# Performance work log

Hardware: AMD Instinct MI355X
Metric: run time of the kernel (lower is better)

The kernel has to match this reference:

```python
import jax, jax.numpy as jnp
import numpy as np

N = 65536          # nodes
E = 1048576        # edges
IN_C = 128
HID_C = 32
HEADS = 4
OUT_C = 64
NEG_SLOPE = 0.2
EPS = 1e-16


def gat_conv(x, edge_index, W, att_src, att_dst, bias, heads, out_c, concat):
    """PyG-style GATConv. x: [N, F_in]; edge_index: [2, E] (row=src, col=dst).
    W: [F_in, heads*out_c]; att_src/att_dst: [heads, out_c]; bias: [heads*out_c] or [out_c]."""
    src, dst = edge_index[0], edge_index[1]
    n = x.shape[0]
    h = (x @ W).reshape(n, heads, out_c)                      # [N, H, C]
    a_src = jnp.einsum('nhc,hc->nh', h, att_src)              # [N, H]
    a_dst = jnp.einsum('nhc,hc->nh', h, att_dst)              # [N, H]
    alpha = a_src[src] + a_dst[dst]                           # [E, H]
    alpha = jax.nn.leaky_relu(alpha, NEG_SLOPE)
    # segment softmax over incoming edges of each destination node
    amax = jax.ops.segment_max(alpha, dst, num_segments=n)    # [N, H]
    alpha = jnp.exp(alpha - amax[dst])
    denom = jax.ops.segment_sum(alpha, dst, num_segments=n)   # [N, H]
    alpha = alpha / (denom[dst] + EPS)
    # weighted scatter-add aggregation
    msgs = alpha[:, :, None] * h[src]                         # [E, H, C]
    out = jax.ops.segment_sum(msgs, dst, num_segments=n)      # [N, H, C]
    if concat:
        out = out.reshape(n, heads * out_c)
    else:
        out = out.mean(axis=1)
    return out + bias


def setup_inputs() -> dict:
    key = jax.random.key(0)
    ks = jax.random.split(key, 10)
    s_in = 1.0 / np.sqrt(IN_C)
    s_h = 1.0 / np.sqrt(HEADS * HID_C)
    x = jax.random.normal(ks[0], (N, IN_C), dtype=jnp.float32)
    edge_index = jax.random.randint(ks[1], (2, E), 0, N, dtype=jnp.int64)
    W1 = jax.random.normal(ks[2], (IN_C, HEADS * HID_C), dtype=jnp.float32) * s_in
    att_src1 = jax.random.normal(ks[3], (HEADS, HID_C), dtype=jnp.float32) * s_h
    att_dst1 = jax.random.normal(ks[4], (HEADS, HID_C), dtype=jnp.float32) * s_h
    b1 = jnp.zeros((HEADS * HID_C,), dtype=jnp.float32)
    W2 = jax.random.normal(ks[5], (HEADS * HID_C, OUT_C), dtype=jnp.float32) * s_h
    att_src2 = jax.random.normal(ks[6], (1, OUT_C), dtype=jnp.float32) * s_h
    att_dst2 = jax.random.normal(ks[7], (1, OUT_C), dtype=jnp.float32) * s_h
    b2 = jnp.zeros((OUT_C,), dtype=jnp.float32)
    return {"x": x, "edge_index": edge_index, "W1": W1, "att_src1": att_src1,
            "att_dst1": att_dst1, "b1": b1, "W2": W2, "att_src2": att_src2,
            "att_dst2": att_dst2, "b2": b2}


def reference(x, edge_index, W1, att_src1, att_dst1, b1, W2, att_src2, att_dst2, b2):
    # dropout is identity in eval mode
    h = gat_conv(x, edge_index, W1, att_src1, att_dst1, b1, HEADS, HID_C, concat=True)
    h = jax.nn.sigmoid(h)
    h = gat_conv(h, edge_index, W2, att_src2, att_dst2, b2, 1, OUT_C, concat=True)
    return jax.nn.sigmoid(h)
```

## Files before the change

kernel.cpp:

```cpp
#include <hip/hip_runtime.h>
#include <hip/hip_fp16.h>

#define N_NODES 65536
#define N_EDGES 1048576
#define NBUCK 256
#define PBLOCKS 1024
#define EPB (N_EDGES / PBLOCKS)
#define K4CAP 6144
#define GB1 (N_NODES / 64)
constexpr float NEG = 0.2f;
constexpr float EPS_ = 1e-16f;
constexpr float WSHIFT = 2.7725887f;

typedef __attribute__((ext_vector_type(8))) short bf16x8;
typedef __attribute__((ext_vector_type(4))) float f32x4;

__device__ __forceinline__ unsigned short f2bf(float f) {
    unsigned int u = __float_as_uint(f);
    return (unsigned short)((u + 0x7fffu + ((u >> 16) & 1u)) >> 16);
}
__device__ __forceinline__ unsigned short f2h(float f) {
    __half_raw r = __half_raw(__float2half(f));
    return r.x;
}
__device__ __forceinline__ __half2 u2h2(unsigned int u) {
    union { unsigned int u; __half2 h; } c; c.u = u; return c.h;
}
__device__ __forceinline__ unsigned int h22u(__half2 h) {
    union { unsigned int u; __half2 h; } c; c.h = h; return c.u;
}
__device__ __forceinline__ float lrelu_exp_s(float l) {
    return __expf(fmaxf(l, NEG * l) - WSHIFT);
}


__global__ __launch_bounds__(1024) void scan_a(const int* __restrict__ in,
                                               int* __restrict__ out,
                                               int* __restrict__ bsum) {
    __shared__ int sm[1024];
    int t = threadIdx.x, i = blockIdx.x * 1024 + t;
    int v = in[i];
    sm[t] = v;
    __syncthreads();
    for (int off = 1; off < 1024; off <<= 1) {
        int u = (t >= off) ? sm[t - off] : 0;
        __syncthreads();
        sm[t] += u;
        __syncthreads();
    }
    out[i] = sm[t] - v;
    if (t == 1023) bsum[blockIdx.x] = sm[t];
}

__global__ __launch_bounds__(1024) void scan_c(int* __restrict__ arr,
                                               const int* __restrict__ bsum) {
    __shared__ int partial[4];
    int t = threadIdx.x;
    if (t < 256) {
        int v = (t < (int)blockIdx.x) ? bsum[t] : 0;
        #pragma unroll
        for (int msk = 1; msk < 64; msk <<= 1) v += __shfl_xor(v, msk);
        if ((t & 63) == 0) partial[t >> 6] = v;
    }
    __syncthreads();
    int pref = partial[0] + partial[1] + partial[2] + partial[3];
    arr[blockIdx.x * 1024 + t] += pref;
}

__global__ __launch_bounds__(256) void partition_kernel(const int* __restrict__ ei,
                                                        const int* __restrict__ cursor_mat,
                                                        unsigned int* __restrict__ edge_part) {
    __shared__ int h[NBUCK];
    __shared__ int start[NBUCK];
    __shared__ int cur[NBUCK];
    __shared__ int gcur[NBUCK];
    __shared__ unsigned int stage[EPB];
    int t = threadIdx.x;
    h[t] = 0;
    gcur[t] = cursor_mat[t * PBLOCKS + blockIdx.x];
    __syncthreads();
    unsigned int ent[EPB / 256];
    int base = blockIdx.x * EPB;
    #pragma unroll
    for (int i = 0; i < EPB / 256; ++i) {
        int e = base + i * 256 + t;
        int s = ei[e], d = ei[N_EDGES + e];
        ent[i] = ((unsigned int)s << 16) | (unsigned int)d;
        atomicAdd(&h[d >> 8], 1);
    }
    __syncthreads();
    int v = h[t];
    start[t] = v;
    __syncthreads();
    for (int off = 1; off < 256; off <<= 1) {
        int u = (t >= off) ? start[t - off] : 0;
        __syncthreads();
        start[t] += u;
        __syncthreads();
    }
    int excl = start[t] - v;
    start[t] = excl;
    cur[t] = excl;
    __syncthreads();
    #pragma unroll
    for (int i = 0; i < EPB / 256; ++i) {
        int b = (int)((ent[i] & 0xffffu) >> 8);
        int slot = atomicAdd(&cur[b], 1);
        stage[slot] = ent[i];
    }
    __syncthreads();
    int s0 = t * (EPB / 256);
    #pragma unroll
    for (int i = 0; i < EPB / 256; ++i) {
        unsigned int p = stage[s0 + i];
        int b = (int)((p & 0xffffu) >> 8);
        edge_part[gcur[b] + (s0 + i - start[b])] = p;
    }
}

__global__ __launch_bounds__(1024) void finalize_kernel(const unsigned int* __restrict__ edge_part,
                                                        const int* __restrict__ cursor_mat,
                                                        int* __restrict__ row_ptr,
                                                        unsigned short* __restrict__ csr16) {
    __shared__ int h[256];
    __shared__ int sc[256];
    __shared__ int cur[256];
    __shared__ unsigned short stage[K4CAP];
    int t = threadIdx.x;
    int b = blockIdx.x;
    if (b == NBUCK - 1 && t == 0) row_ptr[N_NODES] = N_EDGES;
    int cs = cursor_mat[b * PBLOCKS];
    int ce = (b == NBUCK - 1) ? N_EDGES : cursor_mat[(b + 1) * PBLOCKS];
    int cnt = ce - cs;
    if (t < 256) h[t] = 0;
    __syncthreads();
    for (int i = t; i < cnt; i += 1024)
        atomicAdd(&h[edge_part[cs + i] & 0xffu], 1);
    __syncthreads();
    int v = 0;
    if (t < 256) { v = h[t]; sc[t] = v; }
    __syncthreads();
    for (int off = 1; off < 256; off <<= 1) {
        int u = (t < 256 && t >= off) ? sc[t - off] : 0;
        __syncthreads();
        if (t < 256) sc[t] += u;
        __syncthreads();
    }
    if (t < 256) {
        int excl = sc[t] - v;
        row_ptr[b * 256 + t] = cs + excl;
        cur[t] = excl;
    }
    __syncthreads();
    if (cnt <= K4CAP) {
        for (int i = t; i < cnt; i += 1024) {
            unsigned int p = edge_part[cs + i];
            int slot = atomicAdd(&cur[p & 0xffu], 1);
            stage[slot] = (unsigned short)(p >> 16);
        }
        __syncthreads();
        for (int i = t; i < cnt; i += 1024)
            csr16[cs + i] = stage[i];
    } else {
        for (int i = t; i < cnt; i += 1024) {
            unsigned int p = edge_part[cs + i];
            int slot = atomicAdd(&cur[p & 0xffu], 1);
            csr16[cs + slot] = (unsigned short)(p >> 16);
        }
    }
}


__global__ __launch_bounds__(256) void gemm1_hist(const float* __restrict__ X,
                                                  const float* __restrict__ W,
                                                  const float* __restrict__ as_w,
                                                  const float* __restrict__ ad_w,
                                                  const int* __restrict__ ei,
                                                  unsigned short* __restrict__ H,
                                                  float* __restrict__ a_src,
                                                  float* __restrict__ a_dst,
                                                  int* __restrict__ hist_mat) {
    extern __shared__ unsigned short Wl[];
    int t = threadIdx.x;
    if (blockIdx.x >= GB1) {
        int* hs = (int*)Wl;
        int pb = blockIdx.x - GB1;
        hs[t] = 0;
        __syncthreads();
        int base = pb * EPB;
        #pragma unroll
        for (int i = 0; i < EPB / 256; ++i) {
            int d = ei[N_EDGES + base + i * 256 + t];
            atomicAdd(&hs[d >> 8], 1);
        }
        __syncthreads();
        hist_mat[t * PBLOCKS + pb] = hs[t];
        return;
    }
    constexpr int OUTC = 128;
    constexpr int NT = OUTC / 16;
    for (int idx = t; idx < OUTC * 128; idx += 256) {
        int j = idx & 7;
        int ln = (idx >> 3) & 63;
        int fc = idx >> 9;
        int kc = fc & 3, ct = fc >> 2;
        int k = kc * 32 + (ln >> 4) * 8 + j;
        int nn = ct * 16 + (ln & 15);
        Wl[idx] = (unsigned short)f2bf(W[k * OUTC + nn]);
    }
    __syncthreads();
    int wave = t >> 6, lane = t & 63;
    int m = lane & 15, quad = lane >> 4;
    int node_base = blockIdx.x * 64 + wave * 16;
    const float* xrow = X + (size_t)(node_base + m) * 128 + quad * 8;
    bf16x8 a[4];
    #pragma unroll
    for (int kc = 0; kc < 4; ++kc) {
        float4 u = *(const float4*)(xrow + kc * 32);
        float4 v = *(const float4*)(xrow + kc * 32 + 4);
        bf16x8 af;
        af[0] = (short)f2bf(u.x); af[1] = (short)f2bf(u.y);
        af[2] = (short)f2bf(u.z); af[3] = (short)f2bf(u.w);
        af[4] = (short)f2bf(v.x); af[5] = (short)f2bf(v.y);
        af[6] = (short)f2bf(v.z); af[7] = (short)f2bf(v.w);
        a[kc] = af;
    }
    float asv[NT], adv[NT];
    #pragma unroll
    for (int ct = 0; ct < NT; ++ct) {
        asv[ct] = as_w[ct * 16 + m];
        adv[ct] = ad_w[ct * 16 + m];
    }
    float ps[4][4] = {};
    float pd[4][4] = {};
    #pragma unroll
    for (int ct = 0; ct < NT; ++ct) {
        f32x4 acc = {0.f, 0.f, 0.f, 0.f};
        #pragma unroll
        for (int kc = 0; kc < 4; ++kc) {
            bf16x8 bfr = *(const bf16x8*)(Wl + ((ct * 4 + kc) * 64 + lane) * 8);
            acc = __builtin_amdgcn_mfma_f32_16x16x32_bf16(a[kc], bfr, acc, 0, 0, 0);
        }
        int hh = ct >> 1;
        #pragma unroll
        for (int r = 0; r < 4; ++r) {
            H[(size_t)(node_base + quad * 4 + r) * OUTC + ct * 16 + m] = f2h(acc[r]);
            ps[r][hh] += acc[r] * asv[ct];
            pd[r][hh] += acc[r] * adv[ct];
        }
    }
    #pragma unroll
    for (int r = 0; r < 4; ++r) {
        #pragma unroll
        for (int hh = 0; hh < 4; ++hh) {
            float s = ps[r][hh], d = pd[r][hh];
            #pragma unroll
            for (int msk = 1; msk < 16; msk <<= 1) {
                s += __shfl_xor(s, msk);
                d += __shfl_xor(d, msk);
            }
            if (m == 0) {
                int node = node_base + quad * 4 + r;
                a_src[node * 4 + hh] = s;
                a_dst[node * 4 + hh] = d;
            }
        }
    }
}


__global__ __launch_bounds__(256) void gemm2_mfma(const unsigned short* __restrict__ X,
                                                  const float* __restrict__ W,
                                                  const float* __restrict__ as_w,
                                                  const float* __restrict__ ad_w,
                                                  unsigned short* __restrict__ H,
                                                  float* __restrict__ a_src,
                                                  float* __restrict__ a_dst) {
    constexpr int OUTC = 64;
    constexpr int NT = OUTC / 16;
    extern __shared__ unsigned short Wl[];
    int t = threadIdx.x;
    for (int idx = t; idx < OUTC * 128; idx += 256) {
        int j = idx & 7;
        int ln = (idx >> 3) & 63;
        int fc = idx >> 9;
        int kc = fc & 3, ct = fc >> 2;
        int k = kc * 32 + (ln >> 4) * 8 + j;
        int nn = ct * 16 + (ln & 15);
        Wl[idx] = (unsigned short)f2bf(W[k * OUTC + nn]);
    }
    __syncthreads();
    int wave = t >> 6, lane = t & 63;
    int m = lane & 15, quad = lane >> 4;
    int node_base = blockIdx.x * 64 + wave * 16;
    const unsigned short* xrow = X + (size_t)(node_base + m) * 128 + quad * 8;
    bf16x8 a[4];
    #pragma unroll
    for (int kc = 0; kc < 4; ++kc) a[kc] = *(const bf16x8*)(xrow + kc * 32);
    float asv[NT], adv[NT];
    #pragma unroll
    for (int ct = 0; ct < NT; ++ct) {
        asv[ct] = as_w[ct * 16 + m];
        adv[ct] = ad_w[ct * 16 + m];
    }
    float ps[4] = {};
    float pd[4] = {};
    #pragma unroll
    for (int ct = 0; ct < NT; ++ct) {
        f32x4 acc = {0.f, 0.f, 0.f, 0.f};
        #pragma unroll
        for (int kc = 0; kc < 4; ++kc) {
            bf16x8 bfr = *(const bf16x8*)(Wl + ((ct * 4 + kc) * 64 + lane) * 8);
            acc = __builtin_amdgcn_mfma_f32_16x16x32_bf16(a[kc], bfr, acc, 0, 0, 0);
        }
        #pragma unroll
        for (int r = 0; r < 4; ++r) {
            H[(size_t)(node_base + quad * 4 + r) * OUTC + ct * 16 + m] = f2h(acc[r]);
            ps[r] += acc[r] * asv[ct];
            pd[r] += acc[r] * adv[ct];
        }
    }
    #pragma unroll
    for (int r = 0; r < 4; ++r) {
        float s = ps[r], d = pd[r];
        #pragma unroll
        for (int msk = 1; msk < 16; msk <<= 1) {
            s += __shfl_xor(s, msk);
            d += __shfl_xor(d, msk);
        }
        if (m == 0) {
            int node = node_base + quad * 4 + r;
            a_src[node] = s;
            a_dst[node] = d;
        }
    }
}


__global__ __launch_bounds__(256) void agg1_kernel(const int* __restrict__ row_ptr,
                                                   const unsigned short* __restrict__ csr16,
                                                   const unsigned int* __restrict__ h1u,
                                                   const float* __restrict__ a_src,
                                                   const float* __restrict__ a_dst,
                                                   const float* __restrict__ b1,
                                                   unsigned short* __restrict__ x2) {
    int wave = (blockIdx.x * 256 + threadIdx.x) >> 6;
    int lane = threadIdx.x & 63;
    int half = lane >> 5;
    int ln = lane & 31;
    int n = wave * 2 + half;
    int j8 = ln & 7;
    int whead = ln >> 3;
    int sub = ln >> 4;
    int col = ln & 15;
    int hd_c = col >> 2;
    int rbase = half * 32 + hd_c * 8 + sub;
    float adw = a_dst[n * 4 + whead];
    const unsigned int* h1c = h1u + col * 4;
    const float* asw = a_src + whead;
    int e = row_ptr[n], end = row_ptr[n + 1];
    __half2 acc0 = u2h2(0u), acc1 = u2h2(0u), acc2 = u2h2(0u), acc3 = u2h2(0u);
    float denom = 0.f;
    unsigned int cur = 0u;
    if (e < end) {
        int mb = end - e; if (mb > 8) mb = 8;
        int s_l = (int)csr16[e + (j8 < mb ? j8 : 0)];
        float l = asw[s_l * 4] + adw;
        float wv = (j8 < mb) ? lrelu_exp_s(l) : 0.f;
        denom += wv;
        cur = ((unsigned int)f2h(wv) << 16) | (unsigned int)s_l;
    }
    while (e < end) {
        unsigned int pk0 = __shfl(cur, rbase);
        unsigned int pk1 = __shfl(cur, rbase + 2);
        unsigned int pk2 = __shfl(cur, rbase + 4);
        unsigned int pk3 = __shfl(cur, rbase + 6);
        uint4 hv0 = *(const uint4*)(h1c + (size_t)(pk0 & 0xffffu) * 64);
        uint4 hv1 = *(const uint4*)(h1c + (size_t)(pk1 & 0xffffu) * 64);
        uint4 hv2 = *(const uint4*)(h1c + (size_t)(pk2 & 0xffffu) * 64);
        uint4 hv3 = *(const uint4*)(h1c + (size_t)(pk3 & 0xffffu) * 64);
        int en = e + 8;
        unsigned int nxt = 0u;
        if (en < end) {
            int mb = end - en; if (mb > 8) mb = 8;
            int s_l = (int)csr16[en + (j8 < mb ? j8 : 0)];
            float l = asw[s_l * 4] + adw;
            float wv = (j8 < mb) ? lrelu_exp_s(l) : 0.f;
            denom += wv;
            nxt = ((unsigned int)f2h(wv) << 16) | (unsigned int)s_l;
        }
        unsigned int wu; __half2 w2;
        wu = pk0 >> 16; w2 = u2h2(wu | (wu << 16));
        acc0 = __hfma2(w2, u2h2(hv0.x), acc0);
        acc1 = __hfma2(w2, u2h2(hv0.y), acc1);
        acc2 = __hfma2(w2, u2h2(hv0.z), acc2);
        acc3 = __hfma2(w2, u2h2(hv0.w), acc3);
        wu = pk1 >> 16; w2 = u2h2(wu | (wu << 16));
        acc0 = __hfma2(w2, u2h2(hv1.x), acc0);
        acc1 = __hfma2(w2, u2h2(hv1.y), acc1);
        acc2 = __hfma2(w2, u2h2(hv1.z), acc2);
        acc3 = __hfma2(w2, u2h2(hv1.w), acc3);
        wu = pk2 >> 16; w2 = u2h2(wu | (wu << 16));
        acc0 = __hfma2(w2, u2h2(hv2.x), acc0);
        acc1 = __hfma2(w2, u2h2(hv2.y), acc1);
        acc2 = __hfma2(w2, u2h2(hv2.z), acc2);
        acc3 = __hfma2(w2, u2h2(hv2.w), acc3);
        wu = pk3 >> 16; w2 = u2h2(wu | (wu << 16));
        acc0 = __hfma2(w2, u2h2(hv3.x), acc0);
        acc1 = __hfma2(w2, u2h2(hv3.y), acc1);
        acc2 = __hfma2(w2, u2h2(hv3.z), acc2);
        acc3 = __hfma2(w2, u2h2(hv3.w), acc3);
        cur = nxt;
        e = en;
    }
    acc0 = __hadd2(acc0, u2h2(__shfl_xor(h22u(acc0), 16)));
    acc1 = __hadd2(acc1, u2h2(__shfl_xor(h22u(acc1), 16)));
    acc2 = __hadd2(acc2, u2h2(__shfl_xor(h22u(acc2), 16)));
    acc3 = __hadd2(acc3, u2h2(__shfl_xor(h22u(acc3), 16)));
    #pragma unroll
    for (int m = 1; m < 8; m <<= 1) denom += __shfl_xor(denom, m);
    float dfin = __shfl(denom, half * 32 + hd_c * 8);
    if (sub == 0) {
        float inv = 1.f / (dfin + EPS_);
        int c0 = col * 8;
        float v[8];
        v[0] = __low2float(acc0); v[1] = __high2float(acc0);
        v[2] = __low2float(acc1); v[3] = __high2float(acc1);
        v[4] = __low2float(acc2); v[5] = __high2float(acc2);
        v[6] = __low2float(acc3); v[7] = __high2float(acc3);
        unsigned int o[4];
        #pragma unroll
        for (int i = 0; i < 4; ++i) {
            float u0 = v[2 * i] * inv + b1[c0 + 2 * i];
            float u1 = v[2 * i + 1] * inv + b1[c0 + 2 * i + 1];
            u0 = 1.f / (1.f + __expf(-u0));
            u1 = 1.f / (1.f + __expf(-u1));
            o[i] = (unsigned int)f2bf(u0) | ((unsigned int)f2bf(u1) << 16);
        }
        *(uint4*)(x2 + (size_t)n * 128 + c0) = make_uint4(o[0], o[1], o[2], o[3]);
    }
}

__global__ __launch_bounds__(256) void agg2_kernel(const int* __restrict__ row_ptr,
                                                   const unsigned short* __restrict__ csr16,
                                                   const unsigned int* __restrict__ h2u,
                                                   const float* __restrict__ a_src,
                                                   const float* __restrict__ a_dst,
                                                   const float* __restrict__ b2,
                                                   float* __restrict__ out) {
    int wave = (blockIdx.x * 256 + threadIdx.x) >> 6;
    int lane = threadIdx.x & 63;
    int half = lane >> 5;
    int ln = lane & 31;
    int n = wave * 2 + half;
    int j8 = ln & 7;
    int sub = (ln >> 3) & 3;
    int col = ln & 7;
    int rbase = half * 32 + sub;
    float ad = a_dst[n];
    const unsigned int* h2c = h2u + col * 4;
    int e = row_ptr[n], end = row_ptr[n + 1];
    __half2 acc0 = u2h2(0u), acc1 = u2h2(0u), acc2 = u2h2(0u), acc3 = u2h2(0u);
    float denom = 0.f;
    unsigned int cur = 0u;
    if (e < end) {
        int mb = end - e; if (mb > 8) mb = 8;
        int s_l = (int)csr16[e + (j8 < mb ? j8 : 0)];
        float l = a_src[s_l] + ad;
        float wv = (j8 < mb) ? lrelu_exp_s(l) : 0.f;
        denom += wv;
        cur = ((unsigned int)f2h(wv) << 16) | (unsigned int)s_l;
    }
    while (e < end) {
        unsigned int pk0 = __shfl(cur, rbase);
        unsigned int pk1 = __shfl(cur, rbase + 4);
        uint4 hv0 = *(const uint4*)(h2c + (size_t)(pk0 & 0xffffu) * 32);
        uint4 hv1 = *(const uint4*)(h2c + (size_t)(pk1 & 0xffffu) * 32);
        int en = e + 8;
        unsigned int nxt = 0u;
        if (en < end) {
            int mb = end - en; if (mb > 8) mb = 8;
            int s_l = (int)csr16[en + (j8 < mb ? j8 : 0)];
            float l = a_src[s_l] + ad;
            float wv = (j8 < mb) ? lrelu_exp_s(l) : 0.f;
            denom += wv;
            nxt = ((unsigned int)f2h(wv) << 16) | (unsigned int)s_l;
        }
        unsigned int wu; __half2 w2;
        wu = pk0 >> 16; w2 = u2h2(wu | (wu << 16));
        acc0 = __hfma2(w2, u2h2(hv0.x), acc0);
        acc1 = __hfma2(w2, u2h2(hv0.y), acc1);
        acc2 = __hfma2(w2, u2h2(hv0.z), acc2);
        acc3 = __hfma2(w2, u2h2(hv0.w), acc3);
        wu = pk1 >> 16; w2 = u2h2(wu | (wu << 16));
        acc0 = __hfma2(w2, u2h2(hv1.x), acc0);
        acc1 = __hfma2(w2, u2h2(hv1.y), acc1);
        acc2 = __hfma2(w2, u2h2(hv1.z), acc2);
        acc3 = __hfma2(w2, u2h2(hv1.w), acc3);
        cur = nxt;
        e = en;
    }
    #pragma unroll
    for (int m = 8; m < 32; m <<= 1) {
        acc0 = __hadd2(acc0, u2h2(__shfl_xor(h22u(acc0), m)));
        acc1 = __hadd2(acc1, u2h2(__shfl_xor(h22u(acc1), m)));
        acc2 = __hadd2(acc2, u2h2(__shfl_xor(h22u(acc2), m)));
        acc3 = __hadd2(acc3, u2h2(__shfl_xor(h22u(acc3), m)));
    }
    #pragma unroll
    for (int m = 1; m < 8; m <<= 1) denom += __shfl_xor(denom, m);
    if (sub == 0) {
        float inv = 1.f / (denom + EPS_);
        int c0 = col * 8;
        float v[8];
        v[0] = __low2float(acc0); v[1] = __high2float(acc0);
        v[2] = __low2float(acc1); v[3] = __high2float(acc1);
        v[4] = __low2float(acc2); v[5] = __high2float(acc2);
        v[6] = __low2float(acc3); v[7] = __high2float(acc3);
        float o[8];
        #pragma unroll
        for (int i = 0; i < 8; ++i) {
            float u = v[i] * inv + b2[c0 + i];
            o[i] = 1.f / (1.f + __expf(-u));
        }
        float4* dst = (float4*)(out + (size_t)n * 64 + c0);
        dst[0] = make_float4(o[0], o[1], o[2], o[3]);
        dst[1] = make_float4(o[4], o[5], o[6], o[7]);
    }
}


extern "C" void kernel_launch(void* const* d_in, const int* in_sizes, int n_in,
                              void* d_out, int out_size, void* d_ws, size_t ws_size,
                              hipStream_t stream) {
    (void)in_sizes; (void)n_in; (void)out_size; (void)ws_size;
    const float* x   = (const float*)d_in[0];
    const int*   ei  = (const int*)d_in[1];
    const float* W1  = (const float*)d_in[2];
    const float* as1 = (const float*)d_in[3];
    const float* ad1 = (const float*)d_in[4];
    const float* b1  = (const float*)d_in[5];
    const float* W2  = (const float*)d_in[6];
    const float* as2 = (const float*)d_in[7];
    const float* ad2 = (const float*)d_in[8];
    const float* b2  = (const float*)d_in[9];
    float* out = (float*)d_out;

    char* p = (char*)d_ws;
    auto alloc = [&](size_t bytes) -> void* {
        void* r = (void*)p;
        p += (bytes + 255) & ~(size_t)255;
        return r;
    };
    int* hist_mat   = (int*)alloc((size_t)NBUCK * PBLOCKS * 4);
    int* cursor_mat = (int*)alloc((size_t)NBUCK * PBLOCKS * 4);
    int* bsum       = (int*)alloc(256 * 4);
    unsigned int* edge_part = (unsigned int*)alloc((size_t)N_EDGES * 4);
    int* row_ptr    = (int*)alloc((size_t)(N_NODES + 1) * 4);
    unsigned short* csr16 = (unsigned short*)alloc((size_t)N_EDGES * 2);
    unsigned short* h1 = (unsigned short*)alloc((size_t)N_NODES * 128 * 2);
    float* a_src1   = (float*)alloc((size_t)N_NODES * 4 * 4);
    float* a_dst1   = (float*)alloc((size_t)N_NODES * 4 * 4);
    unsigned short* x2 = (unsigned short*)alloc((size_t)N_NODES * 128 * 2);
    unsigned short* h2 = (unsigned short*)alloc((size_t)N_NODES * 64 * 2);
    float* a_src2   = (float*)alloc((size_t)N_NODES * 4);
    float* a_dst2   = (float*)alloc((size_t)N_NODES * 4);

    gemm1_hist<<<GB1 + PBLOCKS, 256, 128 * 128 * 2, stream>>>(
        x, W1, as1, ad1, ei, h1, a_src1, a_dst1, hist_mat);
    scan_a<<<NBUCK * PBLOCKS / 1024, 1024, 0, stream>>>(hist_mat, cursor_mat, bsum);
    scan_c<<<NBUCK * PBLOCKS / 1024, 1024, 0, stream>>>(cursor_mat, bsum);
    partition_kernel<<<PBLOCKS, 256, 0, stream>>>(ei, cursor_mat, edge_part);
    finalize_kernel<<<NBUCK, 1024, 0, stream>>>(edge_part, cursor_mat, row_ptr, csr16);
    agg1_kernel<<<N_NODES / 8, 256, 0, stream>>>(row_ptr, csr16, (const unsigned int*)h1,
                                                 a_src1, a_dst1, b1, x2);
    gemm2_mfma<<<N_NODES / 64, 256, 128 * 64 * 2, stream>>>(x2, W2, as2, ad2, h2, a_src2, a_dst2);
    agg2_kernel<<<N_NODES / 8, 256, 0, stream>>>(row_ptr, csr16, (const unsigned int*)h2,
                                                 a_src2, a_dst2, b2, out);
}
```

Baseline: 221.1 us.

## Fold block-sum scan into consumers and stage GEMM outputs through LDS

Removes the scan_c kernel. partition_kernel and finalize_kernel now each recompute the prefix over the 256 block sums in shared memory and add it to cursor_mat on the fly, which saves a launch and a read-modify-write pass over the cursor matrix. Both GEMM kernels also keep their accumulators in registers, write the fp16 H tile to LDS (reusing the weight buffer after a barrier), and then copy it to global memory with coalesced 16-byte stores instead of scattered 2-byte stores. The cost is a redundant small scan in every partition and finalize block, plus extra barriers and more registers held in the GEMMs.

```diff
diff --git a/kernel.cpp b/kernel.cpp
--- a/kernel.cpp
+++ b/kernel.cpp
@@ -52,32 +52,20 @@
     if (t == 1023) bsum[blockIdx.x] = sm[t];
 }
 
-__global__ __launch_bounds__(1024) void scan_c(int* __restrict__ arr,
-                                               const int* __restrict__ bsum) {
-    __shared__ int partial[4];
-    int t = threadIdx.x;
-    if (t < 256) {
-        int v = (t < (int)blockIdx.x) ? bsum[t] : 0;
-        #pragma unroll
-        for (int msk = 1; msk < 64; msk <<= 1) v += __shfl_xor(v, msk);
-        if ((t & 63) == 0) partial[t >> 6] = v;
-    }
-    __syncthreads();
-    int pref = partial[0] + partial[1] + partial[2] + partial[3];
-    arr[blockIdx.x * 1024 + t] += pref;
-}
-
 __global__ __launch_bounds__(256) void partition_kernel(const int* __restrict__ ei,
                                                         const int* __restrict__ cursor_mat,
+                                                        const int* __restrict__ bsum,
                                                         unsigned int* __restrict__ edge_part) {
     __shared__ int h[NBUCK];
     __shared__ int start[NBUCK];
     __shared__ int cur[NBUCK];
     __shared__ int gcur[NBUCK];
+    __shared__ int bs[NBUCK];
     __shared__ unsigned int stage[EPB];
     int t = threadIdx.x;
     h[t] = 0;
-    gcur[t] = cursor_mat[t * PBLOCKS + blockIdx.x];
+    int bsv = bsum[t];
+    bs[t] = bsv;
     __syncthreads();
     unsigned int ent[EPB / 256];
     int base = blockIdx.x * EPB;
@@ -93,14 +81,17 @@
     start[t] = v;
     __syncthreads();
     for (int off = 1; off < 256; off <<= 1) {
-        int u = (t >= off) ? start[t - off] : 0;
-        __syncthreads();
-        start[t] += u;
+        int u1 = (t >= off) ? start[t - off] : 0;
+        int u2 = (t >= off) ? bs[t - off] : 0;
+        __syncthreads();
+        start[t] += u1;
+        bs[t] += u2;
         __syncthreads();
     }
     int excl = start[t] - v;
     start[t] = excl;
     cur[t] = excl;
+    gcur[t] = cursor_mat[t * PBLOCKS + blockIdx.x] + (bs[t] - bsv);
     __syncthreads();
     #pragma unroll
     for (int i = 0; i < EPB / 256; ++i) {
@@ -120,17 +111,27 @@
 
 __global__ __launch_bounds__(1024) void finalize_kernel(const unsigned int* __restrict__ edge_part,
                                                         const int* __restrict__ cursor_mat,
+                                                        const int* __restrict__ bsum,
                                                         int* __restrict__ row_ptr,
                                                         unsigned short* __restrict__ csr16) {
     __shared__ int h[256];
     __shared__ int sc[256];
     __shared__ int cur[256];
+    __shared__ int bs[256];
     __shared__ unsigned short stage[K4CAP];
     int t = threadIdx.x;
     int b = blockIdx.x;
     if (b == NBUCK - 1 && t == 0) row_ptr[N_NODES] = N_EDGES;
-    int cs = cursor_mat[b * PBLOCKS];
-    int ce = (b == NBUCK - 1) ? N_EDGES : cursor_mat[(b + 1) * PBLOCKS];
+    if (t < 256) bs[t] = bsum[t];
+    __syncthreads();
+    for (int off = 1; off < 256; off <<= 1) {
+        int u = (t < 256 && t >= off) ? bs[t - off] : 0;
+        __syncthreads();
+        if (t < 256) bs[t] += u;
+        __syncthreads();
+    }
+    int cs = cursor_mat[b * PBLOCKS] + (b ? bs[b - 1] : 0);
+    int ce = (b == NBUCK - 1) ? N_EDGES : cursor_mat[(b + 1) * PBLOCKS] + bs[b];
     int cnt = ce - cs;
     if (t < 256) h[t] = 0;
     __syncthreads();
@@ -233,6 +234,7 @@
     }
     float ps[4][4] = {};
     float pd[4][4] = {};
+    f32x4 accs[NT];
     #pragma unroll
     for (int ct = 0; ct < NT; ++ct) {
         f32x4 acc = {0.f, 0.f, 0.f, 0.f};
@@ -241,10 +243,10 @@
             bf16x8 bfr = *(const bf16x8*)(Wl + ((ct * 4 + kc) * 64 + lane) * 8);
             acc = __builtin_amdgcn_mfma_f32_16x16x32_bf16(a[kc], bfr, acc, 0, 0, 0);
         }
+        accs[ct] = acc;
         int hh = ct >> 1;
         #pragma unroll
         for (int r = 0; r < 4; ++r) {
-            H[(size_t)(node_base + quad * 4 + r) * OUTC + ct * 16 + m] = f2h(acc[r]);
             ps[r][hh] += acc[r] * asv[ct];
             pd[r][hh] += acc[r] * adv[ct];
         }
@@ -266,6 +268,21 @@
             }
         }
     }
+    __syncthreads();
+    unsigned short* Hst = Wl;
+    int lrow = wave * 16 + quad * 4;
+    #pragma unroll
+    for (int ct = 0; ct < NT; ++ct) {
+        #pragma unroll
+        for (int r = 0; r < 4; ++r)
+            Hst[(lrow + r) * OUTC + ct * 16 + m] = f2h(accs[ct][r]);
+    }
+    __syncthreads();
+    const uint4* Hsv = (const uint4*)Hst;
+    uint4* Hg = (uint4*)(H + (size_t)blockIdx.x * 64 * OUTC);
+    #pragma unroll
+    for (int i = 0; i < 64 * OUTC / 8 / 256; ++i)
+        Hg[i * 256 + t] = Hsv[i * 256 + t];
 }
 
 
@@ -305,6 +322,7 @@
     }
     float ps[4] = {};
     float pd[4] = {};
+    f32x4 accs[NT];
     #pragma unroll
     for (int ct = 0; ct < NT; ++ct) {
         f32x4 acc = {0.f, 0.f, 0.f, 0.f};
@@ -313,9 +331,9 @@
             bf16x8 bfr = *(const bf16x8*)(Wl + ((ct * 4 + kc) * 64 + lane) * 8);
             acc = __builtin_amdgcn_mfma_f32_16x16x32_bf16(a[kc], bfr, acc, 0, 0, 0);
         }
+        accs[ct] = acc;
         #pragma unroll
         for (int r = 0; r < 4; ++r) {
-            H[(size_t)(node_base + quad * 4 + r) * OUTC + ct * 16 + m] = f2h(acc[r]);
             ps[r] += acc[r] * asv[ct];
             pd[r] += acc[r] * adv[ct];
         }
@@ -334,6 +352,21 @@
             a_dst[node] = d;
         }
     }
+    __syncthreads();
+    unsigned short* Hst = Wl;
+    int lrow = wave * 16 + quad * 4;
+    #pragma unroll
+    for (int ct = 0; ct < NT; ++ct) {
+        #pragma unroll
+        for (int r = 0; r < 4; ++r)
+            Hst[(lrow + r) * OUTC + ct * 16 + m] = f2h(accs[ct][r]);
+    }
+    __syncthreads();
+    const uint4* Hsv = (const uint4*)Hst;
+    uint4* Hg = (uint4*)(H + (size_t)blockIdx.x * 64 * OUTC);
+    #pragma unroll
+    for (int i = 0; i < 64 * OUTC / 8 / 256; ++i)
+        Hg[i * 256 + t] = Hsv[i * 256 + t];
 }
 
 
@@ -569,9 +602,8 @@
     gemm1_hist<<<GB1 + PBLOCKS, 256, 128 * 128 * 2, stream>>>(
         x, W1, as1, ad1, ei, h1, a_src1, a_dst1, hist_mat);
     scan_a<<<NBUCK * PBLOCKS / 1024, 1024, 0, stream>>>(hist_mat, cursor_mat, bsum);
-    scan_c<<<NBUCK * PBLOCKS / 1024, 1024, 0, stream>>>(cursor_mat, bsum);
-    partition_kernel<<<PBLOCKS, 256, 0, stream>>>(ei, cursor_mat, edge_part);
-    finalize_kernel<<<NBUCK, 1024, 0, stream>>>(edge_part, cursor_mat, row_ptr, csr16);
+    partition_kernel<<<PBLOCKS, 256, 0, stream>>>(ei, cursor_mat, bsum, edge_part);
+    finalize_kernel<<<NBUCK, 1024, 0, stream>>>(edge_part, cursor_mat, bsum, row_ptr, csr16);
     agg1_kernel<<<N_NODES / 8, 256, 0, stream>>>(row_ptr, csr16, (const unsigned int*)h1,
                                                  a_src1, a_dst1, b1, x2);
     gemm2_mfma<<<N_NODES / 64, 256, 128 * 64 * 2, stream>>>(x2, W2, as2, ad2, h2, a_src2, a_dst2);
```

Result: no change. 221.0 us (-0.1%).
